# Optimization experiments

Hardware: AMD Instinct MI355X
Metric: run time of the kernel (lower is better)

Reference implementation:

```python
import jax, jax.numpy as jnp
import numpy as np

NUM = 4
EPS = 1e-8


def setup_inputs() -> dict:
    key = jax.random.key(0)
    ks = jax.random.split(key, 8)
    B, N, D = 64, 1024, 512
    x = jax.random.normal(ks[0], (B, N, D), dtype=jnp.float32)
    # marginal priors: valid probability distributions (log is taken inside)
    p0 = jax.nn.softmax(jax.random.normal(ks[1], (B, 1, D), dtype=jnp.float32), axis=2)
    q0 = jax.nn.softmax(jax.random.normal(ks[2], (B, N, 1), dtype=jnp.float32), axis=1)
    # strictly positive regularization weights / ADMM step sizes
    a1 = jax.random.uniform(ks[3], (NUM,), dtype=jnp.float32, minval=0.1, maxval=1.1)
    a2 = jax.random.uniform(ks[4], (NUM,), dtype=jnp.float32, minval=0.1, maxval=1.1)
    a3 = jax.random.uniform(ks[5], (NUM,), dtype=jnp.float32, minval=0.1, maxval=1.1)
    rho = jax.random.uniform(ks[6], (NUM,), dtype=jnp.float32, minval=0.1, maxval=1.1)
    mask = jnp.ones((B, N, 1), dtype=jnp.float32)
    return {"x": x, "p0": p0, "q0": q0, "a1": a1, "a2": a2, "a3": a3,
            "rho": rho, "mask": mask}


def _lse(y, axis):
    return jax.scipy.special.logsumexp(y, axis=axis, keepdims=True)


def _masked_log_colsum(y, mask):
    # stable log(sum_n exp(y)*mask) over axis 1, masking as in the torch code
    ymin = jnp.min(y, axis=1, keepdims=True)
    ymax = jnp.max(ymin - mask * ymin + y, axis=1, keepdims=True)
    lse = jnp.log(jnp.sum(jnp.exp((y - ymax) * mask) * mask, axis=1, keepdims=True))
    return lse, ymax


def uot_badmm(x, p0, q0, a1, a2, a3, rho, mask, num=NUM, eps=EPS):
    log_p0 = jnp.log(p0)                      # (B,1,D)
    log_q0 = jnp.log(q0 + eps) * mask         # (B,N,1)
    log_t = (log_q0 + log_p0) * mask          # (B,N,D)
    log_s = (log_q0 + log_p0) * mask
    log_mu = jnp.log(p0)
    log_eta = jnp.log(q0 + eps) * mask
    z = jnp.zeros_like(log_t)
    z1 = jnp.zeros_like(p0)
    z2 = jnp.zeros_like(q0)
    for k in range(num):
        n = min(k, a1.shape[0] - 1)
        rn = rho[n]
        # t-update
        y = (x - z) / rn + log_s
        log_t = mask * (log_eta - _lse(y, 2)) + y
        # s-update
        y = (z + rn * log_t) / (a1[n] + rn)
        lse, ymax = _masked_log_colsum(y, mask)
        log_s = mask * (log_mu - lse - ymax) + y
        t = jnp.exp(log_t) * mask
        s = jnp.exp(log_s) * mask
        z = z + rn * (t - s)
        # mu-update
        y = (rn * log_mu + a2[n] * log_p0 - z1) / (rn + a2[n])
        log_mu = y - _lse(y, 2)
        # eta-update
        y = (rn * log_eta + a3[n] * log_q0 - z2) / (rn + a3[n])
        lse, ymax = _masked_log_colsum(y, mask)
        log_eta = (y - lse - ymax) * mask
        # dual updates
        z1 = z1 + rn * (jnp.exp(log_mu) - jnp.sum(s, axis=1, keepdims=True))
        z2 = z2 + rn * (jnp.exp(log_eta) * mask - jnp.sum(t, axis=2, keepdims=True)) * mask
    return jnp.exp(log_t) * mask


def reference(x, p0, q0, a1, a2, a3, rho, mask):
    return uot_badmm(x, p0, q0, a1, a2, a3, rho, mask, num=NUM, eps=EPS)
```

## Files before the change

### kernel.cpp

```cpp
#include <hip/hip_runtime.h>
#include <math.h>

#define BB 64
#define NN 1024
#define DD 512
#define SEG 64
#define ROWS_PER_BLOCK 16
#define ROWS_PER_WAVE 4
#define WAVES 4
#define EPSQ 1e-8f
#define L2E 1.44269504088896340736f

typedef _Float16 h8 __attribute__((ext_vector_type(8)));
typedef float f32x4 __attribute__((ext_vector_type(4)));

#if __has_builtin(__builtin_amdgcn_exp2f)
__device__ __forceinline__ float ex2(float x) { return __builtin_amdgcn_exp2f(x); }
#else
__device__ __forceinline__ float ex2(float x) { return exp2f(x); }
#endif
#if __has_builtin(__builtin_amdgcn_logf)
__device__ __forceinline__ float lg2(float x) { return __builtin_amdgcn_logf(x); }
#else
__device__ __forceinline__ float lg2(float x) { return log2f(x); }
#endif

__device__ __forceinline__ float wmax(float v) {
#pragma unroll
    for (int o = 32; o; o >>= 1) v = fmaxf(v, __shfl_xor(v, o));
    return v;
}
__device__ __forceinline__ float wsum(float v) {
#pragma unroll
    for (int o = 32; o; o >>= 1) v += __shfl_xor(v, o);
    return v;
}
template <int NW>
__device__ __forceinline__ float block_max(float v, float* lds) {
    v = wmax(v);
    __syncthreads();
    if ((threadIdx.x & 63) == 0) lds[threadIdx.x >> 6] = v;
    __syncthreads();
    float r = lds[0];
#pragma unroll
    for (int i = 1; i < NW; i++) r = fmaxf(r, lds[i]);
    return r;
}
template <int NW>
__device__ __forceinline__ float block_sum(float v, float* lds) {
    v = wsum(v);
    __syncthreads();
    if ((threadIdx.x & 63) == 0) lds[threadIdx.x >> 6] = v;
    __syncthreads();
    float r = 0.f;
#pragma unroll
    for (int i = 0; i < NW; i++) r += lds[i];
    return r;
}

__device__ __forceinline__ void load8(float* r, const float* p) {
    float4 a = *reinterpret_cast<const float4*>(p);
    float4 b = *reinterpret_cast<const float4*>(p + 4);
    r[0] = a.x; r[1] = a.y; r[2] = a.z; r[3] = a.w;
    r[4] = b.x; r[5] = b.y; r[6] = b.z; r[7] = b.w;
}
__device__ __forceinline__ void load8_nt(float* r, const float* p) {
    f32x4 a = __builtin_nontemporal_load(reinterpret_cast<const f32x4*>(p));
    f32x4 b = __builtin_nontemporal_load(reinterpret_cast<const f32x4*>(p) + 1);
    r[0] = a.x; r[1] = a.y; r[2] = a.z; r[3] = a.w;
    r[4] = b.x; r[5] = b.y; r[6] = b.z; r[7] = b.w;
}
__device__ __forceinline__ void store8_nt(float* p, const float* r) {
    f32x4 a, b;
    a.x = r[0]; a.y = r[1]; a.z = r[2]; a.w = r[3];
    b.x = r[4]; b.y = r[5]; b.z = r[6]; b.w = r[7];
    __builtin_nontemporal_store(a, reinterpret_cast<f32x4*>(p));
    __builtin_nontemporal_store(b, reinterpret_cast<f32x4*>(p) + 1);
}

__global__ __launch_bounds__(512) void small_seq_kernel(
    const float* __restrict__ p0, const float* __restrict__ q0,
    const float* __restrict__ a2, const float* __restrict__ a3,
    const float* __restrict__ rho, float* __restrict__ lmu_seq,
    float* __restrict__ leta_seq, float* __restrict__ lp_tab) {
    __shared__ float lds[8];
    const int b = blockIdx.x, t = threadIdx.x;
    const float lp = lg2(p0[b * DD + t]);
    lp_tab[b * DD + t] = lp;
    const float lqa = lg2(q0[b * NN + t] + EPSQ);
    const float lqb = lg2(q0[b * NN + t + 512] + EPSQ);
    float lmu = lp, lea = lqa, leb = lqb;
    float z1 = 0.f, z2a = 0.f, z2b = 0.f;
    lmu_seq[b * DD + t] = lmu;
    leta_seq[b * NN + t] = lea;
    leta_seq[b * NN + t + 512] = leb;
    for (int k = 0; k < 4; k++) {
        const float r = rho[k], A2 = a2[k], A3 = a3[k];
        const float rL = r * L2E;
        float y = (r * lmu + A2 * lp - z1) / (r + A2);
        float m = block_max<8>(y, lds);
        float S = block_sum<8>(ex2(y - m), lds);
        float lse = m + lg2(S);
        float lmun = y - lse;
        z1 += rL * (ex2(lmun) - ex2(lmu));
        lmu = lmun;
        if (k < 2) lmu_seq[(size_t)(k + 1) * (BB * DD) + b * DD + t] = lmu;
        float ya = (r * lea + A3 * lqa - z2a) / (r + A3);
        float yb = (r * leb + A3 * lqb - z2b) / (r + A3);
        m = block_max<8>(fmaxf(ya, yb), lds);
        S = block_sum<8>(ex2(ya - m) + ex2(yb - m), lds);
        lse = m + lg2(S);
        float lean = ya - lse, lebn = yb - lse;
        z2a += rL * (ex2(lean) - ex2(lea));
        z2b += rL * (ex2(lebn) - ex2(leb));
        lea = lean;
        leb = lebn;
        if (k < 3) {
            leta_seq[(size_t)(k + 1) * (BB * NN) + b * NN + t] = lea;
            leta_seq[(size_t)(k + 1) * (BB * NN) + b * NN + t + 512] = leb;
        }
    }
}

__global__ __launch_bounds__(256, 4) void a0_kernel(
    const float* __restrict__ x, const float* __restrict__ lp_tab,
    const float* __restrict__ leta_seq, _Float16* __restrict__ x16,
    float* __restrict__ crow, float* __restrict__ psum,
    const float* __restrict__ a1, const float* __restrict__ rho) {
    __shared__ float sms[WAVES][DD];
    const int b = blockIdx.x >> 6, seg = blockIdx.x & 63;
    const int w = threadIdx.x >> 6, l = threadIdx.x & 63;
    const int d0 = l * 8;
    const float r0 = rho[0];
    const float inv_r0 = 1.f / r0;
    const float inv_ar0 = 1.f / (a1[0] + r0);

    float lp[8];
    load8(lp, lp_tab + b * DD + d0);
    const float* lrowq = leta_seq + b * NN;

    float ss[8];
#pragma unroll
    for (int j = 0; j < 8; j++) ss[j] = 0.f;

    const int row0 = seg * ROWS_PER_BLOCK + w * ROWS_PER_WAVE;
#pragma unroll 2
    for (int i = 0; i < ROWS_PER_WAVE; i++) {
        const int n = row0 + i;
        const size_t base = ((size_t)b * NN + n) * DD + d0;
        const float lq = lrowq[n];
        float xv[8];
        load8_nt(xv, x + base);
        h8 xh;
#pragma unroll
        for (int j = 0; j < 8; j++) xh[j] = (_Float16)(xv[j] * L2E);
        *reinterpret_cast<h8*>(x16 + base) = xh;
        float yb[8];
        float se = 0.f;
#pragma unroll
        for (int j = 0; j < 8; j++) {
            float xs = (float)xh[j];
            yb[j] = fmaf(xs, inv_r0, lq + lp[j]);
            se += ex2(yb[j]);
        }
        float lse = lg2(wsum(se));
        const float c = lq - lse;
        if (l == 0) crow[b * NN + n] = c;
#pragma unroll
        for (int j = 0; j < 8; j++) {
            float lt = c + yb[j];
            ss[j] += ex2((r0 * lt) * inv_ar0);
        }
    }
#pragma unroll
    for (int j = 0; j < 8; j += 4)
        *reinterpret_cast<float4*>(&sms[w][d0 + j]) =
            make_float4(ss[j], ss[j + 1], ss[j + 2], ss[j + 3]);
    __syncthreads();
    for (int d = threadIdx.x; d < DD; d += 256) {
        float S = sms[0][d] + sms[1][d] + sms[2][d] + sms[3][d];
        psum[((size_t)b * SEG + seg) * DD + d] = S;
    }
}

__global__ __launch_bounds__(256) void colfin_kernel(
    const float* __restrict__ psum, const float* __restrict__ lmu_seq,
    float* __restrict__ cc_tab, int k) {
    const int idx = blockIdx.x * 256 + threadIdx.x;
    const int b = idx >> 9, d = idx & (DD - 1);
    float S = 0.f;
    for (int s = 0; s < SEG; s++)
        S += psum[((size_t)b * SEG + s) * DD + d];
    cc_tab[(size_t)k * (BB * DD) + idx] =
        lmu_seq[(size_t)k * (BB * DD) + idx] - lg2(S);
}

template <int P, bool LAST>
__global__ __launch_bounds__(256, 4) void f_kernel(
    const _Float16* __restrict__ x16, float* __restrict__ out,
    const float* __restrict__ lp_tab, const float* __restrict__ leta_seq,
    float* __restrict__ crow, const float* __restrict__ cc_tab,
    float* __restrict__ psum, const float* __restrict__ a1,
    const float* __restrict__ rho) {
    __shared__ float sms[WAVES][DD];
    const int b = blockIdx.x >> 6, seg = blockIdx.x & 63;
    const int w = threadIdx.x >> 6, l = threadIdx.x & 63;
    const int d0 = l * 8;

    float rv[P + 1], invr[P + 1], rLv[P + 1], invar[P + 1];
#pragma unroll
    for (int i = 0; i <= P; i++) {
        rv[i] = rho[i];
        invr[i] = 1.f / rv[i];
        rLv[i] = rv[i] * L2E;
        invar[i] = 1.f / (a1[i] + rv[i]);
    }

    float lp[8];
    load8(lp, lp_tab + b * DD + d0);
    float ccv[P][8];
#pragma unroll
    for (int i = 0; i < P; i++)
        load8(ccv[i], cc_tab + (size_t)i * (BB * DD) + b * DD + d0);

    const float* lrowq = leta_seq + b * NN;
    const float* lrowP = leta_seq + (size_t)P * (BB * NN) + b * NN;

    float ss[8];
#pragma unroll
    for (int j = 0; j < 8; j++) ss[j] = 0.f;

    const int row0 = seg * ROWS_PER_BLOCK + w * ROWS_PER_WAVE;
#pragma unroll 2
    for (int i0 = 0; i0 < ROWS_PER_WAVE; i0++) {
        const int n = row0 + i0;
        const size_t base = ((size_t)b * NN + n) * DD + d0;
        h8 xh;
        if (LAST)
            xh = __builtin_nontemporal_load(
                reinterpret_cast<const h8*>(x16 + base));
        else
            xh = *reinterpret_cast<const h8*>(x16 + base);
        const float lq = lrowq[n];
        float cr[P];
#pragma unroll
        for (int i = 0; i < P; i++)
            cr[i] = crow[(size_t)i * (BB * NN) + b * NN + n];
        const float letaP = lrowP[n];
        float yb[8], znj[8];
        float se = 0.f;
#pragma unroll
        for (int j = 0; j < 8; j++) {
            float xs = (float)xh[j];
            float y = fmaf(xs, invr[0], lq + lp[j]);
            float lt = cr[0] + y;
            float zn = 0.f;
#pragma unroll
            for (int i = 1; i <= P; i++) {
                float y2v = (zn + rv[i - 1] * lt) * invar[i - 1];
                float ls = ccv[i - 1][j] + y2v;
                zn = zn + rLv[i - 1] * (ex2(lt) - ex2(ls));
                y = fmaf(xs - zn, invr[i], ls);
                if (i < P) lt = cr[i] + y;
            }
            yb[j] = y;
            znj[j] = zn;
            se += ex2(y);
        }
        float lse = lg2(wsum(se));
        const float c = letaP - lse;
        if (LAST) {
            float o[8];
#pragma unroll
            for (int j = 0; j < 8; j++) o[j] = ex2(c + yb[j]);
            store8_nt(out + base, o);
        } else {
            if (l == 0) crow[(size_t)P * (BB * NN) + b * NN + n] = c;
#pragma unroll
            for (int j = 0; j < 8; j++) {
                float lt = c + yb[j];
                float y2P = (znj[j] + rv[P] * lt) * invar[P];
                ss[j] += ex2(y2P);
            }
        }
    }
    if (!LAST) {
#pragma unroll
        for (int j = 0; j < 8; j += 4)
            *reinterpret_cast<float4*>(&sms[w][d0 + j]) =
                make_float4(ss[j], ss[j + 1], ss[j + 2], ss[j + 3]);
        __syncthreads();
        for (int d = threadIdx.x; d < DD; d += 256) {
            float S = sms[0][d] + sms[1][d] + sms[2][d] + sms[3][d];
            psum[((size_t)b * SEG + seg) * DD + d] = S;
        }
    }
}

extern "C" void kernel_launch(void* const* d_in, const int* in_sizes, int n_in,
                              void* d_out, int out_size, void* d_ws,
                              size_t ws_size, hipStream_t stream) {
    (void)in_sizes; (void)n_in; (void)out_size; (void)ws_size;
    const float* x = (const float*)d_in[0];
    const float* p0 = (const float*)d_in[1];
    const float* q0 = (const float*)d_in[2];
    const float* a1 = (const float*)d_in[3];
    const float* a2 = (const float*)d_in[4];
    const float* a3 = (const float*)d_in[5];
    const float* rho = (const float*)d_in[6];
    float* out = (float*)d_out;

    char* w = (char*)d_ws;
    _Float16* x16 = (_Float16*)w;  w += (size_t)BB * NN * DD * 2;
    float* lmu_seq = (float*)w;    w += (size_t)3 * BB * DD * 4;
    float* leta_seq = (float*)w;   w += (size_t)4 * BB * NN * 4;
    float* psum = (float*)w;       w += (size_t)BB * SEG * DD * 4;
    float* cc_tab = (float*)w;     w += (size_t)3 * BB * DD * 4;
    float* crow = (float*)w;       w += (size_t)3 * BB * NN * 4;
    float* lp_tab = (float*)w;

    const int blocks = BB * SEG;
    const int cfin_blocks = (BB * DD) / 256;

    small_seq_kernel<<<BB, 512, 0, stream>>>(p0, q0, a2, a3, rho, lmu_seq,
                                             leta_seq, lp_tab);
    a0_kernel<<<blocks, 256, 0, stream>>>(x, lp_tab, leta_seq, x16, crow, psum,
                                          a1, rho);

    colfin_kernel<<<cfin_blocks, 256, 0, stream>>>(psum, lmu_seq, cc_tab, 0);
    f_kernel<1, false><<<blocks, 256, 0, stream>>>(
        x16, out, lp_tab, leta_seq, crow, cc_tab, psum, a1, rho);

    colfin_kernel<<<cfin_blocks, 256, 0, stream>>>(psum, lmu_seq, cc_tab, 1);
    f_kernel<2, false><<<blocks, 256, 0, stream>>>(
        x16, out, lp_tab, leta_seq, crow, cc_tab, psum, a1, rho);

    colfin_kernel<<<cfin_blocks, 256, 0, stream>>>(psum, lmu_seq, cc_tab, 2);
    f_kernel<3, true><<<blocks, 256, 0, stream>>>(
        x16, out, lp_tab, leta_seq, crow, cc_tab, psum, a1, rho);
}
```

Baseline: 180.1 us.

## Fuse small marginal-sequence kernel into first pass kernel as extra blocks

Merges the small per-batch mu/eta sequence kernel into the first x-pass kernel: the first BB blocks run the sequential marginal updates with 256 threads, and the remaining blocks recompute log(p0) and log(q0) locally instead of reading tables the small kernel wrote. This removes one kernel launch and the serialization between the tiny kernel and the big streaming pass. It also drops the unneeded k=3 iteration, switches x loads from nontemporal to normal, and fully unrolls the row loops. The cost is redundant log2 work per block, plus possible occupancy or register changes from the fused kernel and the full unroll.

```diff
diff --git a/kernel.cpp b/kernel.cpp
--- a/kernel.cpp
+++ b/kernel.cpp
@@ -64,12 +64,6 @@
     r[0] = a.x; r[1] = a.y; r[2] = a.z; r[3] = a.w;
     r[4] = b.x; r[5] = b.y; r[6] = b.z; r[7] = b.w;
 }
-__device__ __forceinline__ void load8_nt(float* r, const float* p) {
-    f32x4 a = __builtin_nontemporal_load(reinterpret_cast<const f32x4*>(p));
-    f32x4 b = __builtin_nontemporal_load(reinterpret_cast<const f32x4*>(p) + 1);
-    r[0] = a.x; r[1] = a.y; r[2] = a.z; r[3] = a.w;
-    r[4] = b.x; r[5] = b.y; r[6] = b.z; r[7] = b.w;
-}
 __device__ __forceinline__ void store8_nt(float* p, const float* r) {
     f32x4 a, b;
     a.x = r[0]; a.y = r[1]; a.z = r[2]; a.w = r[3];
@@ -78,79 +72,104 @@
     __builtin_nontemporal_store(b, reinterpret_cast<f32x4*>(p) + 1);
 }
 
-__global__ __launch_bounds__(512) void small_seq_kernel(
-    const float* __restrict__ p0, const float* __restrict__ q0,
+__global__ __launch_bounds__(256, 4) void k1_kernel(
+    const float* __restrict__ x, const float* __restrict__ p0,
+    const float* __restrict__ q0, const float* __restrict__ a1,
     const float* __restrict__ a2, const float* __restrict__ a3,
-    const float* __restrict__ rho, float* __restrict__ lmu_seq,
-    float* __restrict__ leta_seq, float* __restrict__ lp_tab) {
-    __shared__ float lds[8];
-    const int b = blockIdx.x, t = threadIdx.x;
-    const float lp = lg2(p0[b * DD + t]);
-    lp_tab[b * DD + t] = lp;
-    const float lqa = lg2(q0[b * NN + t] + EPSQ);
-    const float lqb = lg2(q0[b * NN + t + 512] + EPSQ);
-    float lmu = lp, lea = lqa, leb = lqb;
-    float z1 = 0.f, z2a = 0.f, z2b = 0.f;
-    lmu_seq[b * DD + t] = lmu;
-    leta_seq[b * NN + t] = lea;
-    leta_seq[b * NN + t + 512] = leb;
-    for (int k = 0; k < 4; k++) {
-        const float r = rho[k], A2 = a2[k], A3 = a3[k];
-        const float rL = r * L2E;
-        float y = (r * lmu + A2 * lp - z1) / (r + A2);
-        float m = block_max<8>(y, lds);
-        float S = block_sum<8>(ex2(y - m), lds);
-        float lse = m + lg2(S);
-        float lmun = y - lse;
-        z1 += rL * (ex2(lmun) - ex2(lmu));
-        lmu = lmun;
-        if (k < 2) lmu_seq[(size_t)(k + 1) * (BB * DD) + b * DD + t] = lmu;
-        float ya = (r * lea + A3 * lqa - z2a) / (r + A3);
-        float yb = (r * leb + A3 * lqb - z2b) / (r + A3);
-        m = block_max<8>(fmaxf(ya, yb), lds);
-        S = block_sum<8>(ex2(ya - m) + ex2(yb - m), lds);
-        lse = m + lg2(S);
-        float lean = ya - lse, lebn = yb - lse;
-        z2a += rL * (ex2(lean) - ex2(lea));
-        z2b += rL * (ex2(lebn) - ex2(leb));
-        lea = lean;
-        leb = lebn;
-        if (k < 3) {
-            leta_seq[(size_t)(k + 1) * (BB * NN) + b * NN + t] = lea;
-            leta_seq[(size_t)(k + 1) * (BB * NN) + b * NN + t + 512] = leb;
-        }
-    }
-}
-
-__global__ __launch_bounds__(256, 4) void a0_kernel(
-    const float* __restrict__ x, const float* __restrict__ lp_tab,
-    const float* __restrict__ leta_seq, _Float16* __restrict__ x16,
-    float* __restrict__ crow, float* __restrict__ psum,
-    const float* __restrict__ a1, const float* __restrict__ rho) {
+    const float* __restrict__ rho, _Float16* __restrict__ x16,
+    float* __restrict__ lmu_seq, float* __restrict__ leta_seq,
+    float* __restrict__ lp_tab, float* __restrict__ crow,
+    float* __restrict__ psum) {
     __shared__ float sms[WAVES][DD];
-    const int b = blockIdx.x >> 6, seg = blockIdx.x & 63;
-    const int w = threadIdx.x >> 6, l = threadIdx.x & 63;
+    __shared__ float s_red[8];
+    const int tid = threadIdx.x;
+
+    if (blockIdx.x < BB) {
+        const int b = blockIdx.x;
+        const float lpA = lg2(p0[b * DD + tid]);
+        const float lpB = lg2(p0[b * DD + tid + 256]);
+        lp_tab[b * DD + tid] = lpA;
+        lp_tab[b * DD + tid + 256] = lpB;
+        float lqv[4], lev[4], z2v[4];
+#pragma unroll
+        for (int u = 0; u < 4; u++) {
+            lqv[u] = lg2(q0[b * NN + tid + 256 * u] + EPSQ);
+            lev[u] = lqv[u];
+            z2v[u] = 0.f;
+            leta_seq[b * NN + tid + 256 * u] = lqv[u];
+        }
+        float lmuA = lpA, lmuB = lpB, z1A = 0.f, z1B = 0.f;
+        lmu_seq[b * DD + tid] = lmuA;
+        lmu_seq[b * DD + tid + 256] = lmuB;
+        for (int k = 0; k < 3; k++) {
+            const float r = rho[k], A2 = a2[k], A3 = a3[k];
+            const float rL = r * L2E;
+            float yA = (r * lmuA + A2 * lpA - z1A) / (r + A2);
+            float yB = (r * lmuB + A2 * lpB - z1B) / (r + A2);
+            float m = block_max<4>(fmaxf(yA, yB), s_red);
+            float S = block_sum<4>(ex2(yA - m) + ex2(yB - m), s_red);
+            float lse = m + lg2(S);
+            float lmuAn = yA - lse, lmuBn = yB - lse;
+            z1A += rL * (ex2(lmuAn) - ex2(lmuA));
+            z1B += rL * (ex2(lmuBn) - ex2(lmuB));
+            lmuA = lmuAn;
+            lmuB = lmuBn;
+            if (k < 2) {
+                lmu_seq[(size_t)(k + 1) * (BB * DD) + b * DD + tid] = lmuA;
+                lmu_seq[(size_t)(k + 1) * (BB * DD) + b * DD + tid + 256] = lmuB;
+            }
+            float yv[4];
+            float ml = -INFINITY;
+#pragma unroll
+            for (int u = 0; u < 4; u++) {
+                yv[u] = (r * lev[u] + A3 * lqv[u] - z2v[u]) / (r + A3);
+                ml = fmaxf(ml, yv[u]);
+            }
+            m = block_max<4>(ml, s_red);
+            float se = 0.f;
+#pragma unroll
+            for (int u = 0; u < 4; u++) se += ex2(yv[u] - m);
+            S = block_sum<4>(se, s_red);
+            lse = m + lg2(S);
+#pragma unroll
+            for (int u = 0; u < 4; u++) {
+                float ln = yv[u] - lse;
+                z2v[u] += rL * (ex2(ln) - ex2(lev[u]));
+                lev[u] = ln;
+                leta_seq[(size_t)(k + 1) * (BB * NN) + b * NN + tid + 256 * u] = ln;
+            }
+        }
+        return;
+    }
+
+    const int blk = blockIdx.x - BB;
+    const int b = blk >> 6, seg = blk & 63;
+    const int w = tid >> 6, l = tid & 63;
     const int d0 = l * 8;
     const float r0 = rho[0];
     const float inv_r0 = 1.f / r0;
     const float inv_ar0 = 1.f / (a1[0] + r0);
 
     float lp[8];
-    load8(lp, lp_tab + b * DD + d0);
-    const float* lrowq = leta_seq + b * NN;
+    {
+        float tmp[8];
+        load8(tmp, p0 + b * DD + d0);
+#pragma unroll
+        for (int j = 0; j < 8; j++) lp[j] = lg2(tmp[j]);
+    }
 
     float ss[8];
 #pragma unroll
     for (int j = 0; j < 8; j++) ss[j] = 0.f;
 
     const int row0 = seg * ROWS_PER_BLOCK + w * ROWS_PER_WAVE;
-#pragma unroll 2
+#pragma unroll
     for (int i = 0; i < ROWS_PER_WAVE; i++) {
         const int n = row0 + i;
         const size_t base = ((size_t)b * NN + n) * DD + d0;
-        const float lq = lrowq[n];
+        const float lq = lg2(q0[b * NN + n] + EPSQ);
         float xv[8];
-        load8_nt(xv, x + base);
+        load8(xv, x + base);
         h8 xh;
 #pragma unroll
         for (int j = 0; j < 8; j++) xh[j] = (_Float16)(xv[j] * L2E);
@@ -177,7 +196,7 @@
         *reinterpret_cast<float4*>(&sms[w][d0 + j]) =
             make_float4(ss[j], ss[j + 1], ss[j + 2], ss[j + 3]);
     __syncthreads();
-    for (int d = threadIdx.x; d < DD; d += 256) {
+    for (int d = tid; d < DD; d += 256) {
         float S = sms[0][d] + sms[1][d] + sms[2][d] + sms[3][d];
         psum[((size_t)b * SEG + seg) * DD + d] = S;
     }
@@ -231,7 +250,7 @@
     for (int j = 0; j < 8; j++) ss[j] = 0.f;
 
     const int row0 = seg * ROWS_PER_BLOCK + w * ROWS_PER_WAVE;
-#pragma unroll 2
+#pragma unroll
     for (int i0 = 0; i0 < ROWS_PER_WAVE; i0++) {
         const int n = row0 + i0;
         const size_t base = ((size_t)b * NN + n) * DD + d0;
@@ -322,10 +341,9 @@
     const int blocks = BB * SEG;
     const int cfin_blocks = (BB * DD) / 256;
 
-    small_seq_kernel<<<BB, 512, 0, stream>>>(p0, q0, a2, a3, rho, lmu_seq,
-                                             leta_seq, lp_tab);
-    a0_kernel<<<blocks, 256, 0, stream>>>(x, lp_tab, leta_seq, x16, crow, psum,
-                                          a1, rho);
+    k1_kernel<<<BB + blocks, 256, 0, stream>>>(x, p0, q0, a1, a2, a3, rho, x16,
+                                               lmu_seq, leta_seq, lp_tab, crow,
+                                               psum);
 
     colfin_kernel<<<cfin_blocks, 256, 0, stream>>>(psum, lmu_seq, cc_tab, 0);
     f_kernel<1, false><<<blocks, 256, 0, stream>>>(
```

Measured after the change: 159.3 us. -11.6%, faster.
